# Performance work log

Measured on AMD Instinct MI355X. Metric: run time of the kernel, lower is better.

Reference implementation:

```python
import jax, jax.numpy as jnp
import numpy as np

NUM_HEADS = 12

def _get_rel_pos(size, rel_pos):
    # q_size == k_size == size, no interpolation needed (table has 2*size-1 rows)
    idx = jnp.arange(size)[:, None] - jnp.arange(size)[None, :] + (size - 1)  # (size,size)
    return rel_pos[idx]  # (size, size, head_dim)

def setup_inputs() -> dict:
    key = jax.random.key(0)
    ks = jax.random.split(key, 7)
    B, H, W, dim = 8, 32, 32, 768
    head_dim = dim // NUM_HEADS
    return {
        "x": jax.random.normal(ks[0], (B, H, W, dim), jnp.float32),
        "qkv_w": jax.random.normal(ks[1], (dim, 3 * dim), jnp.float32) * 0.02,
        "qkv_b": jax.random.normal(ks[2], (3 * dim,), jnp.float32) * 0.02,
        "proj_w": jax.random.normal(ks[3], (dim, dim), jnp.float32) * 0.02,
        "proj_b": jax.random.normal(ks[4], (dim,), jnp.float32) * 0.02,
        "rel_pos_h": jax.random.normal(ks[5], (2 * H - 1, head_dim), jnp.float32) * 0.02,
        "rel_pos_w": jax.random.normal(ks[6], (2 * W - 1, head_dim), jnp.float32) * 0.02,
    }

def reference(x, qkv_w, qkv_b, proj_w, proj_b, rel_pos_h, rel_pos_w):
    B, H, W, dim = x.shape
    N = H * W
    head_dim = dim // NUM_HEADS
    scale = head_dim ** (-0.5)

    qkv = x.reshape(B, N, dim) @ qkv_w + qkv_b                     # (B,N,3*dim)
    qkv = qkv.reshape(B, N, 3, NUM_HEADS, head_dim)
    qkv = qkv.transpose(2, 0, 3, 1, 4).reshape(3, B * NUM_HEADS, N, head_dim)
    q, k, v = qkv[0], qkv[1], qkv[2]                               # (B*h, N, hd)

    attn = jnp.einsum("bnd,bmd->bnm", q * scale, k)                # (B*h, N, N)

    # decomposed relative position bias
    Rh = _get_rel_pos(H, rel_pos_h)                                # (H,H,hd)
    Rw = _get_rel_pos(W, rel_pos_w)                                # (W,W,hd)
    r_q = q.reshape(B * NUM_HEADS, H, W, head_dim)
    rel_h = jnp.einsum("bhwc,hkc->bhwk", r_q, Rh)                  # (B*h,H,W,H)
    rel_w = jnp.einsum("bhwc,wkc->bhwk", r_q, Rw)                  # (B*h,H,W,W)
    attn = (attn.reshape(B * NUM_HEADS, H, W, H, W)
            + rel_h[:, :, :, :, None]
            + rel_w[:, :, :, None, :]).reshape(B * NUM_HEADS, N, N)

    attn = jax.nn.softmax(attn, axis=-1)
    out = jnp.einsum("bnm,bmd->bnd", attn, v)                      # (B*h, N, hd)
    out = out.reshape(B, NUM_HEADS, H, W, head_dim).transpose(0, 2, 3, 1, 4).reshape(B, H, W, dim)
    return out @ proj_w + proj_b
```

## Files before the change

kernel.cpp:

```cpp
#include <hip/hip_runtime.h>
#include <hip/hip_bf16.h>
#include <math.h>

#define DIM   768
#define NHEAD 12
#define NQ    1024

typedef short  short8  __attribute__((ext_vector_type(8)));
typedef unsigned short us8 __attribute__((ext_vector_type(8)));
typedef float  f32x16  __attribute__((ext_vector_type(16)));

#if __has_builtin(__builtin_amdgcn_exp2f)
#define EXP2(x) __builtin_amdgcn_exp2f(x)
#else
#define EXP2(x) __expf(0.69314718056f * (x))
#endif
#define LOG2E 1.44269504089f

__device__ inline ushort f2b(float f) {
  union { float f; unsigned u; } c; c.f = f;
  unsigned r = (c.u + 0x7FFFu + ((c.u >> 16) & 1u)) >> 16;
  return (ushort)r;
}
__device__ inline float b2f(ushort h) {
  union { unsigned u; float f; } c; c.u = ((unsigned)h) << 16;
  return c.f;
}
__device__ inline ushort4 cvt4(float4 v) {
  ushort4 o; o.x = f2b(v.x); o.y = f2b(v.y); o.z = f2b(v.z); o.w = f2b(v.w);
  return o;
}
__device__ inline unsigned pkr(float a, float b) {
  union { float f; unsigned u; } ca, cb; ca.f = a; cb.f = b;
  return __builtin_amdgcn_perm(cb.u + 0x8000u, ca.u + 0x8000u, 0x07060302u);
}
__device__ __forceinline__ void gload16(const void* g, void* l) {
  __builtin_amdgcn_global_load_lds(
      (const __attribute__((address_space(1))) void*)g,
      (__attribute__((address_space(3))) void*)l, 16, 0, 0);
}

__global__ __launch_bounds__(256) void prep(
    const float* __restrict__ x, const float* __restrict__ qkv_w,
    const float* __restrict__ proj_w, ushort* __restrict__ Xb,
    ushort* __restrict__ Wqt, ushort* __restrict__ Wpt) {
  __shared__ ushort Ts[64][68];
  const int blk = blockIdx.x, tid = threadIdx.x;
  if (blk < 768) {
    const float4* src = (const float4*)x;
    ushort4* dst = (ushort4*)Xb;
    int base = blk * 2048;
#pragma unroll
    for (int it = 0; it < 8; ++it) {
      int i = base + it * 256 + tid;
      dst[i] = cvt4(src[i]);
    }
    return;
  }
  const float* W; ushort* Wt; int ncols, tk, tn;
  if (blk < 1200) { int t = blk - 768;  W = qkv_w; Wt = Wqt; ncols = 2304; tk = t % 12; tn = t / 12; }
  else            { int t = blk - 1200; W = proj_w; Wt = Wpt; ncols = 768; tk = t % 12; tn = t / 12; }
  const int kb = tk * 64, nb = tn * 64;
#pragma unroll
  for (int rr = 0; rr < 4; ++rr) {
    int r = (tid >> 4) + rr * 16, c4 = (tid & 15) * 4;
    float4 w = *(const float4*)(W + (size_t)(kb + r) * ncols + nb + c4);
    *(ushort4*)&Ts[r][c4] = cvt4(w);
  }
  __syncthreads();
#pragma unroll
  for (int wwi = 0; wwi < 2; ++wwi) {
    int n = (tid >> 3) + wwi * 32, k8 = (tid & 7) * 8;
    us8 v;
#pragma unroll
    for (int j = 0; j < 8; ++j) v[j] = Ts[k8 + j][n];
    *(us8*)(Wt + (size_t)(nb + n) * 768 + kb + k8) = v;
  }
}

template <int OUTBF>
__global__ __launch_bounds__(256, 4) void gemm_mfma(
    const ushort* __restrict__ A, const ushort* __restrict__ BT,
    const float* __restrict__ bias, void* __restrict__ Cp, int Nc,
    ushort* __restrict__ VTg) {
  __shared__ __align__(16) ushort As[128 * 64];
  __shared__ __align__(16) ushort Bs[128 * 64];
  const int tid = threadIdx.x;
  const int bm = blockIdx.y * 128, bn = blockIdx.x * 128;
  const int lane = tid & 63, wv = tid >> 6;
  const int l31 = lane & 31, lh = lane >> 5;
  const int wm = (wv >> 1) * 64, wn = (wv & 1) * 64;
  const int xr = l31 & 7;

  const int dr = lane >> 3;
  const int ccol = ((lane & 7) ^ dr) * 8;
  const ushort* ag = A + (size_t)(bm + wv * 32 + dr) * 768 + ccol;
  const ushort* bg = BT + (size_t)(bn + wv * 32 + dr) * 768 + ccol;
  ushort* al = &As[wv * 32 * 64];
  ushort* bl = &Bs[wv * 32 * 64];

  f32x16 acc[2][2];
#pragma unroll
  for (int i = 0; i < 2; ++i)
#pragma unroll
    for (int j = 0; j < 2; ++j)
#pragma unroll
      for (int r = 0; r < 16; ++r) acc[i][j][r] = 0.f;

  for (int kt = 0; kt < 768; kt += 64) {
    __syncthreads();
#pragma unroll
    for (int wi = 0; wi < 4; ++wi) {
      gload16(ag + kt + wi * (8 * 768), al + wi * 512);
      gload16(bg + kt + wi * (8 * 768), bl + wi * 512);
    }
    __syncthreads();
#pragma unroll
    for (int ks = 0; ks < 4; ++ks) {
      const int ca = ((ks * 2 + lh) ^ xr) * 8;
      short8 a0 = *(const short8*)&As[(wm + l31) * 64 + ca];
      short8 a1 = *(const short8*)&As[(wm + 32 + l31) * 64 + ca];
      short8 b0 = *(const short8*)&Bs[(wn + l31) * 64 + ca];
      short8 b1 = *(const short8*)&Bs[(wn + 32 + l31) * 64 + ca];
      acc[0][0] = __builtin_amdgcn_mfma_f32_32x32x16_bf16(a0, b0, acc[0][0], 0, 0, 0);
      acc[0][1] = __builtin_amdgcn_mfma_f32_32x32x16_bf16(a0, b1, acc[0][1], 0, 0, 0);
      acc[1][0] = __builtin_amdgcn_mfma_f32_32x32x16_bf16(a1, b0, acc[1][0], 0, 0, 0);
      acc[1][1] = __builtin_amdgcn_mfma_f32_32x32x16_bf16(a1, b1, acc[1][1], 0, 0, 0);
    }
  }

  const bool vreg = OUTBF && (bn >= 1536);
  if (!vreg) {
#pragma unroll
    for (int mb = 0; mb < 2; ++mb)
#pragma unroll
      for (int nb = 0; nb < 2; ++nb) {
        int col = bn + wn + nb * 32 + l31;
        float bv = bias[col];
#pragma unroll
        for (int reg = 0; reg < 16; ++reg) {
          int row = bm + wm + mb * 32 + (reg & 3) + 8 * (reg >> 2) + 4 * lh;
          float o = acc[mb][nb][reg] + bv;
          if (OUTBF) ((ushort*)Cp)[(size_t)row * Nc + col] = f2b(o);
          else       ((float*)Cp)[(size_t)row * Nc + col] = o;
        }
      }
  } else {
    const int b_ = bm >> 10;
    const int nbase = (bm & 1023) + wm;
#pragma unroll
    for (int nb = 0; nb < 2; ++nb) {
      int col = bn + wn + nb * 32 + l31;
      float bv = bias[col];
      int hd_ = col - 1536;
      int h_ = hd_ >> 6, d_ = hd_ & 63;
      ushort* vrow = VTg + ((size_t)(b_ * NHEAD + h_) * 64 + d_) * NQ;
#pragma unroll
      for (int mb = 0; mb < 2; ++mb)
#pragma unroll
        for (int g = 0; g < 4; ++g) {
          int n = nbase + mb * 32 + 8 * g + 4 * lh;
          ushort4 st;
          st.x = f2b(acc[mb][nb][4 * g + 0] + bv);
          st.y = f2b(acc[mb][nb][4 * g + 1] + bv);
          st.z = f2b(acc[mb][nb][4 * g + 2] + bv);
          st.w = f2b(acc[mb][nb][4 * g + 3] + bv);
          *(ushort4*)(vrow + n) = st;
        }
    }
  }
}

__global__ __launch_bounds__(256) void bias_kernel(
    const ushort* __restrict__ QKV, const float* __restrict__ rph,
    const float* __restrict__ rpw, ushort* __restrict__ RH,
    ushort* __restrict__ RW) {
  __shared__ ushort Qb[128][72];
  __shared__ ushort Tb[63][72];

  const int tid = threadIdx.x;
  const int bh = blockIdx.x;
  const int gy = blockIdx.y;
  const int b = bh / NHEAD, h = bh % NHEAD;
  const bool isH = gy < 8;
  const int g4 = isH ? gy : (gy - 8);
  const int lane = tid & 63, wv = tid >> 6;
  const int l31 = lane & 31, lh = lane >> 5;

  const ushort* qb = QKV + (size_t)b * NQ * 2304 + h * 64;
  const float* tab = isH ? rph : rpw;

#pragma unroll
  for (int it = 0; it < 4; ++it) {
    int item = tid + 256 * it;
    if (item < 63 * 16) {
      int r = item >> 4, q4 = (item & 15) * 4;
      float4 v = *(const float4*)(tab + r * 64 + q4);
      *(ushort4*)&Tb[r][q4] = cvt4(v);
    }
  }
#pragma unroll
  for (int it = 0; it < 4; ++it) {
    int item = tid + 256 * it;
    int r = item >> 3, c8 = (item & 7) * 8;
    int n = isH ? (g4 * 128 + r) : ((r & 31) * 32 + g4 * 4 + (r >> 5));
    *(us8*)&Qb[r][c8] = *(const us8*)(qb + (size_t)n * 2304 + c8);
  }
  __syncthreads();

  const int fixed = g4 * 4 + wv;
  f32x16 acc;
#pragma unroll
  for (int i = 0; i < 16; ++i) acc[i] = 0.f;
#pragma unroll
  for (int ks = 0; ks < 4; ++ks) {
    short8 a  = *(const short8*)&Qb[wv * 32 + l31][ks * 16 + lh * 8];
    short8 bb = *(const short8*)&Tb[fixed + 31 - l31][ks * 16 + lh * 8];
    acc = __builtin_amdgcn_mfma_f32_32x32x16_bf16(a, bb, acc, 0, 0, 0);
  }
  ushort* outp = isH ? RH : RW;
#pragma unroll
  for (int reg = 0; reg < 16; ++reg) {
    int row = (reg & 3) + 8 * (reg >> 2) + 4 * lh;
    int n = isH ? (fixed * 32 + row) : (row * 32 + fixed);
    outp[((size_t)bh * NQ + n) * 32 + l31] = f2b(acc[reg] * LOG2E);
  }
}

__global__ __launch_bounds__(256, 3) void attn_mfma(
    const ushort* __restrict__ QKV, const ushort* __restrict__ VTg,
    const ushort* __restrict__ RH, const ushort* __restrict__ RW,
    ushort* __restrict__ O) {
  __shared__ ushort Qs[128][72];
  __shared__ __align__(16) ushort Ks[64 * 64];
  __shared__ __align__(16) ushort VT[64 * 64];

  const int tid = threadIdx.x;
  const int bh = blockIdx.x % 96;
  const int qt = blockIdx.x / 96;
  const int b = bh / NHEAD, h = bh % NHEAD;
  const int n0 = qt * 128;
  const int lane = tid & 63, wv = tid >> 6;
  const int l31 = lane & 31, lh = lane >> 5;
  const int wb = wv * 32;
  const int xr = l31 & 7;

  const ushort* qb = QKV + (size_t)b * NQ * 2304 + h * 64;
  const ushort* kb = qb + DIM;
  const ushort* vtg = VTg + (size_t)bh * 64 * NQ;

#pragma unroll
  for (int it = 0; it < 4; ++it) {
    int item = tid + 256 * it;
    int r = item >> 3, c8 = (item & 7) * 8;
    *(us8*)&Qs[r][c8] = *(const us8*)(qb + (size_t)(n0 + r) * 2304 + c8);
  }

  const int q = n0 + wb + l31;
  const ushort* rwrow = RW + ((size_t)bh * NQ + q) * 32;
  float rwv[16];
#pragma unroll
  for (int g = 0; g < 4; ++g) {
    ushort4 v = *(const ushort4*)(rwrow + 8 * g + 4 * lh);
    rwv[4 * g + 0] = b2f(v.x); rwv[4 * g + 1] = b2f(v.y);
    rwv[4 * g + 2] = b2f(v.z); rwv[4 * g + 3] = b2f(v.w);
  }
  const ushort* rhrow = RH + ((size_t)bh * NQ + q) * 32;

  const int dr = lane >> 3;
  const int ccol = ((lane & 7) ^ dr) * 8;
  const ushort* kg = kb + (size_t)(wv * 16 + dr) * 2304 + ccol;
  const ushort* vg = vtg + (size_t)(wv * 16 + dr) * NQ + ccol;
  ushort* kl = &Ks[wv * 16 * 64];
  ushort* vl = &VT[wv * 16 * 64];

  __syncthreads();
  short8 aq[4];
#pragma unroll
  for (int ks = 0; ks < 4; ++ks)
    aq[ks] = *(const short8*)&Qs[wb + l31][ks * 16 + lh * 8];

  ushort* Pb2 = &Qs[0][0] + wv * (32 * 40);

  f32x16 oacc0, oacc1;
#pragma unroll
  for (int i = 0; i < 16; ++i) { oacc0[i] = 0.f; oacc1[i] = 0.f; }
  float lacc = 0.f;

  for (int t = 0; t < 16; ++t) {
    const int kt = t * 64;
    __syncthreads();
    const unsigned rhu = *(const unsigned*)(rhrow + 2 * t);
    gload16(kg + (size_t)kt * 2304,              kl);
    gload16(kg + (size_t)kt * 2304 + 8 * 2304,   kl + 512);
    gload16(vg + kt,                             vl);
    gload16(vg + kt + 8 * NQ,                    vl + 512);
    __syncthreads();

    const float rh0 = b2f((ushort)(rhu & 0xFFFF));
    const float rh1 = b2f((ushort)(rhu >> 16));

#pragma unroll
    for (int cb = 0; cb < 2; ++cb) {
      f32x16 s;
#pragma unroll
      for (int i = 0; i < 16; ++i) s[i] = 0.f;
#pragma unroll
      for (int ks = 0; ks < 4; ++ks) {
        const int ck = ((ks * 2 + lh) ^ xr) * 8;
        short8 ak = *(const short8*)&Ks[(cb * 32 + l31) * 64 + ck];
        s = __builtin_amdgcn_mfma_f32_32x32x16_bf16(ak, aq[ks], s, 0, 0, 0);
      }
      const float rhv = cb ? rh1 : rh0;
#pragma unroll
      for (int g = 0; g < 4; ++g) {
        float p0 = EXP2(fmaf(s[4 * g + 0], 0.18033688f, rwv[4 * g + 0] + rhv));
        float p1 = EXP2(fmaf(s[4 * g + 1], 0.18033688f, rwv[4 * g + 1] + rhv));
        float p2 = EXP2(fmaf(s[4 * g + 2], 0.18033688f, rwv[4 * g + 2] + rhv));
        float p3 = EXP2(fmaf(s[4 * g + 3], 0.18033688f, rwv[4 * g + 3] + rhv));
        lacc += (p0 + p1) + (p2 + p3);
        uint2 pk; pk.x = pkr(p0, p1); pk.y = pkr(p2, p3);
        *(uint2*)&Pb2[l31 * 40 + 8 * g + 4 * lh] = pk;
      }
#pragma unroll
      for (int ks = 0; ks < 2; ++ks) {
        const int cv = ((cb * 4 + ks * 2 + lh) ^ xr) * 8;
        short8 ap  = *(const short8*)&Pb2[l31 * 40 + ks * 16 + lh * 8];
        short8 bv0 = *(const short8*)&VT[l31 * 64 + cv];
        short8 bv1 = *(const short8*)&VT[(32 + l31) * 64 + cv];
        oacc0 = __builtin_amdgcn_mfma_f32_32x32x16_bf16(ap, bv0, oacc0, 0, 0, 0);
        oacc1 = __builtin_amdgcn_mfma_f32_32x32x16_bf16(ap, bv1, oacc1, 0, 0, 0);
      }
    }
  }

  lacc += __shfl_xor(lacc, 32);
  const float linv = 1.0f / lacc;
  ushort* ob = O + ((size_t)b * NQ + n0 + wb) * DIM + h * 64;
#pragma unroll
  for (int reg = 0; reg < 16; ++reg) {
    int row = (reg & 3) + 8 * (reg >> 2) + 4 * lh;
    float lq = __shfl(linv, row);
    ob[(size_t)row * DIM + l31]      = f2b(oacc0[reg] * lq);
    ob[(size_t)row * DIM + 32 + l31] = f2b(oacc1[reg] * lq);
  }
}

extern "C" void kernel_launch(void* const* d_in, const int* in_sizes, int n_in,
                              void* d_out, int out_size, void* d_ws, size_t ws_size,
                              hipStream_t stream) {
  const float* x      = (const float*)d_in[0];
  const float* qkv_w  = (const float*)d_in[1];
  const float* qkv_b  = (const float*)d_in[2];
  const float* proj_w = (const float*)d_in[3];
  const float* proj_b = (const float*)d_in[4];
  const float* rel_h  = (const float*)d_in[5];
  const float* rel_w  = (const float*)d_in[6];
  float* out = (float*)d_out;

  ushort* qkvb = (ushort*)d_ws;
  ushort* obuf = qkvb + (size_t)8192 * 2304;
  ushort* RH   = obuf + (size_t)8192 * DIM;
  ushort* RW   = RH + (size_t)96 * NQ * 32;
  ushort* Xb   = RW + (size_t)96 * NQ * 32;
  ushort* Wqt  = Xb + (size_t)8192 * DIM;
  ushort* Wpt  = Wqt + (size_t)2304 * DIM;
  ushort* VTg  = Wpt + (size_t)DIM * DIM;

  prep<<<dim3(1344), 256, 0, stream>>>(x, qkv_w, proj_w, Xb, Wqt, Wpt);

  gemm_mfma<1><<<dim3(2304 / 128, 8192 / 128), 256, 0, stream>>>(
      Xb, Wqt, qkv_b, qkvb, 2304, VTg);

  bias_kernel<<<dim3(96, 16), 256, 0, stream>>>(qkvb, rel_h, rel_w, RH, RW);

  attn_mfma<<<dim3(96 * 8), 256, 0, stream>>>(qkvb, VTg, RH, RW, obuf);

  gemm_mfma<0><<<dim3(768 / 128, 8192 / 128), 256, 0, stream>>>(
      obuf, Wpt, proj_b, out, 768, nullptr);
}
```

Measured before the change: 207.6 us.

## Fuse relative-position bias computation into attention kernel, drop bias_kernel

Removes the separate bias kernel and its RH/RW global buffers. Each attention block now loads the rel_pos tables into the shared K/V buffers, computes the height and width bias terms with MFMA against its own Q tile, and keeps them in shared memory and registers. It also merges the K and V shared arrays into one and raises the launch-bounds occupancy hint from 3 to 4. The aim is to save a kernel launch plus global writes and reads of the bias tensors. The cost is extra prologue work and syncs per block, plus possible register pressure at the higher occupancy.

```diff
diff --git a/kernel.cpp b/kernel.cpp
--- a/kernel.cpp
+++ b/kernel.cpp
@@ -171,69 +171,15 @@
   }
 }
 
-__global__ __launch_bounds__(256) void bias_kernel(
-    const ushort* __restrict__ QKV, const float* __restrict__ rph,
-    const float* __restrict__ rpw, ushort* __restrict__ RH,
-    ushort* __restrict__ RW) {
-  __shared__ ushort Qb[128][72];
-  __shared__ ushort Tb[63][72];
-
-  const int tid = threadIdx.x;
-  const int bh = blockIdx.x;
-  const int gy = blockIdx.y;
-  const int b = bh / NHEAD, h = bh % NHEAD;
-  const bool isH = gy < 8;
-  const int g4 = isH ? gy : (gy - 8);
-  const int lane = tid & 63, wv = tid >> 6;
-  const int l31 = lane & 31, lh = lane >> 5;
-
-  const ushort* qb = QKV + (size_t)b * NQ * 2304 + h * 64;
-  const float* tab = isH ? rph : rpw;
-
-#pragma unroll
-  for (int it = 0; it < 4; ++it) {
-    int item = tid + 256 * it;
-    if (item < 63 * 16) {
-      int r = item >> 4, q4 = (item & 15) * 4;
-      float4 v = *(const float4*)(tab + r * 64 + q4);
-      *(ushort4*)&Tb[r][q4] = cvt4(v);
-    }
-  }
-#pragma unroll
-  for (int it = 0; it < 4; ++it) {
-    int item = tid + 256 * it;
-    int r = item >> 3, c8 = (item & 7) * 8;
-    int n = isH ? (g4 * 128 + r) : ((r & 31) * 32 + g4 * 4 + (r >> 5));
-    *(us8*)&Qb[r][c8] = *(const us8*)(qb + (size_t)n * 2304 + c8);
-  }
-  __syncthreads();
-
-  const int fixed = g4 * 4 + wv;
-  f32x16 acc;
-#pragma unroll
-  for (int i = 0; i < 16; ++i) acc[i] = 0.f;
-#pragma unroll
-  for (int ks = 0; ks < 4; ++ks) {
-    short8 a  = *(const short8*)&Qb[wv * 32 + l31][ks * 16 + lh * 8];
-    short8 bb = *(const short8*)&Tb[fixed + 31 - l31][ks * 16 + lh * 8];
-    acc = __builtin_amdgcn_mfma_f32_32x32x16_bf16(a, bb, acc, 0, 0, 0);
-  }
-  ushort* outp = isH ? RH : RW;
-#pragma unroll
-  for (int reg = 0; reg < 16; ++reg) {
-    int row = (reg & 3) + 8 * (reg >> 2) + 4 * lh;
-    int n = isH ? (fixed * 32 + row) : (row * 32 + fixed);
-    outp[((size_t)bh * NQ + n) * 32 + l31] = f2b(acc[reg] * LOG2E);
-  }
-}
-
-__global__ __launch_bounds__(256, 3) void attn_mfma(
+__global__ __launch_bounds__(256, 4) void attn_mfma(
     const ushort* __restrict__ QKV, const ushort* __restrict__ VTg,
-    const ushort* __restrict__ RH, const ushort* __restrict__ RW,
+    const float* __restrict__ rph, const float* __restrict__ rpw,
     ushort* __restrict__ O) {
   __shared__ ushort Qs[128][72];
-  __shared__ __align__(16) ushort Ks[64 * 64];
-  __shared__ __align__(16) ushort VT[64 * 64];
+  __shared__ __align__(16) ushort KV[2 * 64 * 64];
+
+  ushort* const Ksp = KV;
+  ushort* const VTp = KV + 64 * 64;
 
   const int tid = threadIdx.x;
   const int bh = blockIdx.x % 96;
@@ -255,32 +201,90 @@
     int r = item >> 3, c8 = (item & 7) * 8;
     *(us8*)&Qs[r][c8] = *(const us8*)(qb + (size_t)(n0 + r) * 2304 + c8);
   }
-
-  const int q = n0 + wb + l31;
-  const ushort* rwrow = RW + ((size_t)bh * NQ + q) * 32;
-  float rwv[16];
-#pragma unroll
-  for (int g = 0; g < 4; ++g) {
-    ushort4 v = *(const ushort4*)(rwrow + 8 * g + 4 * lh);
-    rwv[4 * g + 0] = b2f(v.x); rwv[4 * g + 1] = b2f(v.y);
-    rwv[4 * g + 2] = b2f(v.z); rwv[4 * g + 3] = b2f(v.w);
-  }
-  const ushort* rhrow = RH + ((size_t)bh * NQ + q) * 32;
+#pragma unroll
+  for (int it = 0; it < 4; ++it) {
+    int item = tid + 256 * it;
+    int r = item >> 4, c4 = (item & 15) * 4;
+    if (r < 63) {
+      float4 vh = *(const float4*)(rph + r * 64 + c4);
+      vh.x *= LOG2E; vh.y *= LOG2E; vh.z *= LOG2E; vh.w *= LOG2E;
+      *(ushort4*)&Ksp[r * 64 + c4] = cvt4(vh);
+      float4 vw = *(const float4*)(rpw + r * 64 + c4);
+      vw.x *= LOG2E; vw.y *= LOG2E; vw.z *= LOG2E; vw.w *= LOG2E;
+      *(ushort4*)&VTp[r * 64 + c4] = cvt4(vw);
+    } else {
+      ushort4 z = {0, 0, 0, 0};
+      *(ushort4*)&Ksp[r * 64 + c4] = z;
+      *(ushort4*)&VTp[r * 64 + c4] = z;
+    }
+  }
 
   const int dr = lane >> 3;
   const int ccol = ((lane & 7) ^ dr) * 8;
   const ushort* kg = kb + (size_t)(wv * 16 + dr) * 2304 + ccol;
   const ushort* vg = vtg + (size_t)(wv * 16 + dr) * NQ + ccol;
-  ushort* kl = &Ks[wv * 16 * 64];
-  ushort* vl = &VT[wv * 16 * 64];
+  ushort* kl = &Ksp[wv * 16 * 64];
+  ushort* vl = &VTp[wv * 16 * 64];
 
   __syncthreads();
+
   short8 aq[4];
 #pragma unroll
   for (int ks = 0; ks < 4; ++ks)
     aq[ks] = *(const short8*)&Qs[wb + l31][ks * 16 + lh * 8];
 
+  __syncthreads();
+
   ushort* Pb2 = &Qs[0][0] + wv * (32 * 40);
+  ushort* rhs = &Qs[0][0] + 5120;
+
+  {
+    const int hq31 = qt * 4 + wv + 31;
+    f32x16 sh;
+#pragma unroll
+    for (int i = 0; i < 16; ++i) sh[i] = 0.f;
+#pragma unroll
+    for (int ks = 0; ks < 4; ++ks) {
+      short8 at = *(const short8*)&Ksp[(hq31 - l31) * 64 + ks * 16 + lh * 8];
+      sh = __builtin_amdgcn_mfma_f32_32x32x16_bf16(at, aq[ks], sh, 0, 0, 0);
+    }
+#pragma unroll
+    for (int reg = 0; reg < 16; ++reg) {
+      int hk = (reg & 3) + 8 * (reg >> 2) + 4 * lh;
+      rhs[hk * 128 + wb + l31] = f2b(sh[reg]);
+    }
+  }
+
+  float rwv[16];
+  {
+    short8 at[8];
+#pragma unroll
+    for (int ub = 0; ub < 2; ++ub)
+#pragma unroll
+      for (int ks = 0; ks < 4; ++ks)
+        at[ub * 4 + ks] =
+            *(const short8*)&VTp[(ub * 32 + l31) * 64 + ks * 16 + lh * 8];
+    f32x16 su0, su1;
+#pragma unroll
+    for (int i = 0; i < 16; ++i) { su0[i] = 0.f; su1[i] = 0.f; }
+#pragma unroll
+    for (int ks = 0; ks < 4; ++ks) {
+      su0 = __builtin_amdgcn_mfma_f32_32x32x16_bf16(at[ks],     aq[ks], su0, 0, 0, 0);
+      su1 = __builtin_amdgcn_mfma_f32_32x32x16_bf16(at[4 + ks], aq[ks], su1, 0, 0, 0);
+    }
+    __syncthreads();
+#pragma unroll
+    for (int reg = 0; reg < 16; ++reg) {
+      int rm = (reg & 3) + 8 * (reg >> 2) + 4 * lh;
+      KV[rm * 128 + wb + l31]        = f2b(su0[reg]);
+      KV[(32 + rm) * 128 + wb + l31] = f2b(su1[reg]);
+    }
+#pragma unroll
+    for (int reg = 0; reg < 16; ++reg) {
+      int rm = (reg & 3) + 8 * (reg >> 2) + 4 * lh;
+      rwv[reg] = b2f(KV[(31 + l31 - rm) * 128 + wb + l31]);
+    }
+  }
 
   f32x16 oacc0, oacc1;
 #pragma unroll
@@ -290,15 +294,14 @@
   for (int t = 0; t < 16; ++t) {
     const int kt = t * 64;
     __syncthreads();
-    const unsigned rhu = *(const unsigned*)(rhrow + 2 * t);
     gload16(kg + (size_t)kt * 2304,              kl);
     gload16(kg + (size_t)kt * 2304 + 8 * 2304,   kl + 512);
     gload16(vg + kt,                             vl);
     gload16(vg + kt + 8 * NQ,                    vl + 512);
     __syncthreads();
 
-    const float rh0 = b2f((ushort)(rhu & 0xFFFF));
-    const float rh1 = b2f((ushort)(rhu >> 16));
+    const float rh0 = b2f(rhs[(2 * t) * 128 + wb + l31]);
+    const float rh1 = b2f(rhs[(2 * t + 1) * 128 + wb + l31]);
 
 #pragma unroll
     for (int cb = 0; cb < 2; ++cb) {
@@ -308,7 +311,7 @@
 #pragma unroll
       for (int ks = 0; ks < 4; ++ks) {
         const int ck = ((ks * 2 + lh) ^ xr) * 8;
-        short8 ak = *(const short8*)&Ks[(cb * 32 + l31) * 64 + ck];
+        short8 ak = *(const short8*)&Ksp[(cb * 32 + l31) * 64 + ck];
         s = __builtin_amdgcn_mfma_f32_32x32x16_bf16(ak, aq[ks], s, 0, 0, 0);
       }
       const float rhv = cb ? rh1 : rh0;
@@ -326,8 +329,8 @@
       for (int ks = 0; ks < 2; ++ks) {
         const int cv = ((cb * 4 + ks * 2 + lh) ^ xr) * 8;
         short8 ap  = *(const short8*)&Pb2[l31 * 40 + ks * 16 + lh * 8];
-        short8 bv0 = *(const short8*)&VT[l31 * 64 + cv];
-        short8 bv1 = *(const short8*)&VT[(32 + l31) * 64 + cv];
+        short8 bv0 = *(const short8*)&VTp[l31 * 64 + cv];
+        short8 bv1 = *(const short8*)&VTp[(32 + l31) * 64 + cv];
         oacc0 = __builtin_amdgcn_mfma_f32_32x32x16_bf16(ap, bv0, oacc0, 0, 0, 0);
         oacc1 = __builtin_amdgcn_mfma_f32_32x32x16_bf16(ap, bv1, oacc1, 0, 0, 0);
       }
@@ -360,9 +363,7 @@
 
   ushort* qkvb = (ushort*)d_ws;
   ushort* obuf = qkvb + (size_t)8192 * 2304;
-  ushort* RH   = obuf + (size_t)8192 * DIM;
-  ushort* RW   = RH + (size_t)96 * NQ * 32;
-  ushort* Xb   = RW + (size_t)96 * NQ * 32;
+  ushort* Xb   = obuf + (size_t)8192 * DIM;
   ushort* Wqt  = Xb + (size_t)8192 * DIM;
   ushort* Wpt  = Wqt + (size_t)2304 * DIM;
   ushort* VTg  = Wpt + (size_t)DIM * DIM;
@@ -372,9 +373,7 @@
   gemm_mfma<1><<<dim3(2304 / 128, 8192 / 128), 256, 0, stream>>>(
       Xb, Wqt, qkv_b, qkvb, 2304, VTg);
 
-  bias_kernel<<<dim3(96, 16), 256, 0, stream>>>(qkvb, rel_h, rel_w, RH, RW);
-
-  attn_mfma<<<dim3(96 * 8), 256, 0, stream>>>(qkvb, VTg, RH, RW, obuf);
+  attn_mfma<<<dim3(96 * 8), 256, 0, stream>>>(qkvb, VTg, rel_h, rel_w, obuf);
 
   gemm_mfma<0><<<dim3(768 / 128, 8192 / 128), 256, 0, stream>>>(
       obuf, Wpt, proj_b, out, 768, nullptr);
```

New measurement: 206.9 us. Within noise of the previous version (-0.3%).
